# Kernel optimization log

Hardware: AMD Instinct MI355X
Metric: run time of the kernel (lower is better)

Reference implementation:

```python
import jax, jax.numpy as jnp
import numpy as np

H = W = 160  # grid mesh -> N = 25600 vertices
B = 4
D = 64


def _grid_mesh(h, w):
    """Triangulated grid; returns symmetric directed edge list (e0, e1), lexicographically
    sorted like np.where(adj > 0) in the original module."""
    idx = np.arange(h * w).reshape(h, w)
    v00 = idx[:-1, :-1].ravel(); v01 = idx[:-1, 1:].ravel()
    v10 = idx[1:, :-1].ravel(); v11 = idx[1:, 1:].ravel()
    faces = np.concatenate([np.stack([v00, v01, v11], 1), np.stack([v00, v11, v10], 1)], 0)
    pairs = np.concatenate([faces[:, [0, 1]], faces[:, [1, 2]], faces[:, [0, 2]]], 0)
    pairs = np.concatenate([pairs, pairs[:, ::-1]], 0)  # symmetrize (adj + adj.T)
    pairs = np.unique(pairs, axis=0)
    return pairs[:, 0].astype(np.int32), pairs[:, 1].astype(np.int32)


def setup_inputs() -> dict:
    key = jax.random.key(0)
    k1, k2 = jax.random.split(key)
    N = H * W
    e0, e1 = _grid_mesh(H, W)
    x = jax.random.normal(k1, (B, N, 3), dtype=jnp.float32)
    J = jax.random.normal(k2, (B, 3 * N, D), dtype=jnp.float32)
    return {"x": x, "J": J, "e0": jnp.asarray(e0), "e1": jnp.asarray(e1), "k": 0}


def _skew(v):
    # cross-product matrix [v]_x : [E,3,3]
    z = jnp.zeros_like(v[:, 0])
    return jnp.stack([
        jnp.stack([z, -v[:, 2], v[:, 1]], -1),
        jnp.stack([v[:, 2], z, -v[:, 0]], -1),
        jnp.stack([-v[:, 1], v[:, 0], z], -1)], -2)


def _arap_single(xi, Ji, e0, e1, deg):
    N = xi.shape[0]
    Dd = Ji.shape[-1]
    J3 = Ji.reshape(N, 3, Dd)           # per-node 3xD blocks of J
    v = xi[e0] - xi[e1]                  # edge vectors [E,3]
    # (2L kron I3) @ J with L = D - A (edge weights 1), coalesce == scatter-add
    nb = jnp.zeros_like(J3).at[e0].add(J3[e1])
    LJ = 2.0 * (deg[:, None, None] * J3 - nb)
    JTLJ = jnp.einsum('ncd,nce->de', J3, LJ)
    # B has block [v]_x at (e0,e1) and accumulated [v]_x at (e0,e0); B^T blocks are -[v]_x
    S = _skew(v)                         # [E,3,3]
    SJ = jnp.einsum('eij,ejd->eid', S, J3[e0])
    BTJ = jnp.zeros_like(J3).at[e1].add(-SJ).at[e0].add(-SJ)
    # C: block-diagonal, per-node sum over outgoing edges of (|v|^2 I - v v^T), then 3x3 inverse
    I3 = jnp.eye(3, dtype=xi.dtype)
    Cb = (v * v).sum(-1)[:, None, None] * I3 - v[:, :, None] * v[:, None, :]
    C = jnp.zeros((N, 3, 3), xi.dtype).at[e0].add(Cb)
    Cinv = jnp.linalg.inv(C)
    CBTJ = jnp.einsum('nij,njd->nid', Cinv, BTJ)
    JTBCBTJ = jnp.einsum('ncd,nce->de', BTJ, CBTJ)
    e = jnp.clip(jnp.linalg.eigvalsh(JTLJ - JTBCBTJ), 0.0)
    pos = e > 0
    # sqrt(clip(e,0)) with a guard so the vjp stays finite at clipped zeros
    return jnp.where(pos, jnp.sqrt(jnp.where(pos, e, 1.0)), 0.0).sum()


def reference(x, J, e0, e1, k):
    N = x.shape[1]
    deg = jnp.zeros((N,), x.dtype).at[e0].add(1.0)
    traces = jax.vmap(lambda xi, Ji: _arap_single(xi, Ji, e0, e1, deg))(x, J)
    return traces.mean()
```

## Files before the change

kernel.cpp:

```cpp
#include <hip/hip_runtime.h>

constexpr int BN = 4;
constexpr int NV = 25600;
constexpr int DD = 64;
constexpr int PP = 72;
constexpr int KP = 34;
constexpr int WW = 160;
constexpr int NPART = 8;
constexpr size_t GEOM_OFF = 1u << 20;
constexpr int GREC = 36;
constexpr int GXN  = 256;
constexpr int NCH  = NV / 4;
constexpr int NITER = NCH / GXN;
static_assert(NITER * GXN == NCH, "grid must divide chunks");

constexpr int NS_STEPS = 11;
__constant__ const float S_TAB[NS_STEPS]  = {1.999940f, 1.999730f, 1.998790f, 1.994560f,
                                             1.976020f, 1.900200f, 1.653000f, 1.241700f,
                                             1.024220f, 1.000220f, 1.000000f};
__constant__ const float MU_TAB[NS_STEPS] = {1.414192f, 1.414118f, 1.413786f, 1.412289f,
                                             1.405710f, 1.378478f, 1.285690f, 1.114316f,
                                             1.012038f, 1.000110f, 1.000000f};

typedef __attribute__((ext_vector_type(8))) short short8;
typedef __attribute__((ext_vector_type(4))) float floatx4;

__device__ __forceinline__ unsigned short f2bf(float x) {
    unsigned u = __float_as_uint(x);
    u += 0x7fffu + ((u >> 16) & 1u);
    return (unsigned short)(u >> 16);
}
__device__ __forceinline__ float bf2f(unsigned short h) {
    return __uint_as_float(((unsigned)h) << 16);
}
__device__ __forceinline__ unsigned pack2bf(float a, float b) {
    return (unsigned)f2bf(a) | ((unsigned)f2bf(b) << 16);
}

__device__ __forceinline__ void mm_arith(int n, int* mm) {
    const int r = n / WW;
    const int c = n - r * WW;
    const bool up = r > 0, dn = r < WW - 1, lf = c > 0, rt = c < WW - 1;
    mm[0] = (up && lf) ? n - WW - 1 : n;
    mm[1] = up ? n - WW : n;
    mm[2] = lf ? n - 1 : n;
    mm[3] = rt ? n + 1 : n;
    mm[4] = dn ? n + WW : n;
    mm[5] = (dn && rt) ? n + WW + 1 : n;
}

__global__ void rowptr_kernel(const int* __restrict__ e0, int E, int* __restrict__ row_ptr,
                              float* __restrict__ M, float* __restrict__ out) {
    const int i = blockIdx.x * blockDim.x + threadIdx.x;
    const int nthr = gridDim.x * blockDim.x;
    for (int j = i; j < NPART * BN * 4096; j += nthr) M[j] = 0.f;
    if (i == 0) out[0] = 0.f;
    if (i > NV) return;
    int lo = 0, hi = E;
    while (lo < hi) {
        int mid = (lo + hi) >> 1;
        if (e0[mid] < i) lo = mid + 1; else hi = mid;
    }
    row_ptr[i] = lo;
}

__global__ __launch_bounds__(256) void geom_kernel(
    const float* __restrict__ x, float* __restrict__ geom,
    float* __restrict__ M, float* __restrict__ out)
{
    const int gid = blockIdx.x * 256 + threadIdx.x;
    for (int i = gid; i < NPART * BN * 4096; i += BN * NV) M[i] = 0.f;
    if (gid == 0) out[0] = 0.f;
    if (gid >= BN * NV) return;
    const int b = gid / NV;
    const int n = gid - b * NV;
    int mm[6];
    mm_arith(n, mm);

    const float* xb = x + (size_t)b * NV * 3;
    const float xn0 = xb[n * 3], xn1 = xb[n * 3 + 1], xn2 = xb[n * 3 + 2];
    float v[6][3];
    float sv0 = 0, sv1 = 0, sv2 = 0;
    float cxx = 0, cxy = 0, cxz = 0, cyy = 0, cyz = 0, czz = 0;
#pragma unroll
    for (int k = 0; k < 6; k++) {
        const int m = mm[k];
        const float v0 = xn0 - xb[m * 3];
        const float v1 = xn1 - xb[m * 3 + 1];
        const float v2 = xn2 - xb[m * 3 + 2];
        v[k][0] = v0; v[k][1] = v1; v[k][2] = v2;
        sv0 += v0; sv1 += v1; sv2 += v2;
        const float s2 = v0 * v0 + v1 * v1 + v2 * v2;
        cxx += s2 - v0 * v0; cyy += s2 - v1 * v1; czz += s2 - v2 * v2;
        cxy -= v0 * v1; cxz -= v0 * v2; cyz -= v1 * v2;
    }
    const float co00 = cyy * czz - cyz * cyz;
    const float co01 = cxz * cyz - cxy * czz;
    const float co02 = cxy * cyz - cxz * cyy;
    const float det  = cxx * co00 + cxy * co01 + cxz * co02;
    const float id   = 1.0f / det;
    const float i00 = co00 * id, i01 = co01 * id, i02 = co02 * id;
    const float i11 = (cxx * czz - cxz * cxz) * id;
    const float i12 = (cxz * cxy - cxx * cyz) * id;
    const float i22 = (cxx * cyy - cxy * cxy) * id;

    float4* g4 = (float4*)(geom + (size_t)gid * GREC);
    g4[0] = make_float4(v[0][0], v[0][1], v[0][2], v[1][0]);
    g4[1] = make_float4(v[1][1], v[1][2], v[2][0], v[2][1]);
    g4[2] = make_float4(v[2][2], v[3][0], v[3][1], v[3][2]);
    g4[3] = make_float4(v[4][0], v[4][1], v[4][2], v[5][0]);
    g4[4] = make_float4(v[5][1], v[5][2], sv0, sv1);
    g4[5] = make_float4(sv2, i00, i01, i02);
    g4[6] = make_float4(i11, i12, i22, 0.f);
    g4[7] = make_float4(__int_as_float(mm[0]), __int_as_float(mm[1]),
                        __int_as_float(mm[2]), __int_as_float(mm[3]));
    g4[8] = make_float4(__int_as_float(mm[4]), __int_as_float(mm[5]), 0.f, 0.f);
}

__device__ __forceinline__ short8 ldfrag(const unsigned short* a, int row, int quad) {
    const unsigned* p = (const unsigned*)(a + row * KP + quad * 8);
    union { unsigned u[4]; short8 s; } t;
    t.u[0] = p[0]; t.u[1] = p[1]; t.u[2] = p[2]; t.u[3] = p[3];
    return t.s;
}

struct GRec { float v[18]; float sv[3]; float ci[6]; };
struct JRegs { float n0, n1, n2; float m0[6], m1[6], m2[6]; };

__device__ __forceinline__ void load_grec(const float* __restrict__ g, GRec& o) {
#pragma unroll
    for (int i = 0; i < 18; i++) o.v[i] = g[i];
    o.sv[0] = g[18]; o.sv[1] = g[19]; o.sv[2] = g[20];
#pragma unroll
    for (int i = 0; i < 6; i++) o.ci[i] = g[21 + i];
}

__device__ __forceinline__ void load_jregs(const float* __restrict__ Jb, int n,
                                           const int* __restrict__ mm, int lane, JRegs& o) {
    const float* Jn = Jb + (size_t)n * (3 * DD) + lane;
    o.n0 = Jn[0]; o.n1 = Jn[DD]; o.n2 = Jn[2 * DD];
#pragma unroll
    for (int k = 0; k < 6; k++) {
        const float* Jm = Jb + (size_t)mm[k] * (3 * DD) + lane;
        o.m0[k] = Jm[0]; o.m1[k] = Jm[DD]; o.m2[k] = Jm[2 * DD];
    }
}

__global__ __launch_bounds__(256, 4) void node_kernel_fast(
    const float* __restrict__ J, const float* __restrict__ geom,
    float* __restrict__ M)
{
    const int b    = blockIdx.y;
    const int w    = __builtin_amdgcn_readfirstlane(threadIdx.x >> 6);
    const int lane = threadIdx.x & 63;
    const int quad = lane >> 4;
    const int mrow = lane & 15;
    const int r0   = w * 16;

    __shared__ unsigned short ATh[2][64 * KP];
    __shared__ unsigned short BTh[2][64 * KP];
    for (int i = threadIdx.x; i < 2 * 64 * KP; i += 256) {
        (&ATh[0][0])[i] = 0;
        (&BTh[0][0])[i] = 0;
    }

    const floatx4 zero4 = {0.f, 0.f, 0.f, 0.f};
    floatx4 accM[4];
#pragma unroll
    for (int c = 0; c < 4; c++) accM[c] = zero4;

    const float* Jb = J + (size_t)b * 3 * NV * DD;
    const float* Gb = geom + (size_t)b * NV * GREC;

    GRec G0, G1;
    JRegs JA, JB;
    {
        const int n0 = blockIdx.x * 4 + w;
        int mm0[6];
        mm_arith(n0, mm0);
        load_jregs(Jb, n0, mm0, lane, JA);
        load_grec(Gb + (size_t)n0 * GREC, G0);
    }
    __syncthreads();

    auto body = [&](int it, const GRec& Gc, const JRegs& Jc, GRec& Gn, JRegs& Jnx) {
        const int p   = it & 1;
        const int itN = (it + 1 < NITER) ? (it + 1) : 0;
        const int nN  = (blockIdx.x + itN * GXN) * 4 + w;
        int mmN[6];
        mm_arith(nN, mmN);
        load_jregs(Jb, nN, mmN, lane, Jnx);
        load_grec(Gb + (size_t)nN * GREC, Gn);

        const float sm0 = (Jc.m0[0] + Jc.m0[1]) + (Jc.m0[2] + Jc.m0[3]) + (Jc.m0[4] + Jc.m0[5]);
        const float sm1 = (Jc.m1[0] + Jc.m1[1]) + (Jc.m1[2] + Jc.m1[3]) + (Jc.m1[4] + Jc.m1[5]);
        const float sm2 = (Jc.m2[0] + Jc.m2[1]) + (Jc.m2[2] + Jc.m2[3]) + (Jc.m2[4] + Jc.m2[5]);
        const float lj0 = 12.f * Jc.n0 - 2.f * sm0;
        const float lj1 = 12.f * Jc.n1 - 2.f * sm1;
        const float lj2 = 12.f * Jc.n2 - 2.f * sm2;

        const float sv0 = Gc.sv[0], sv1 = Gc.sv[1], sv2 = Gc.sv[2];
        float bt0 = sv2 * Jc.n1 - sv1 * Jc.n2;
        float bt1 = sv0 * Jc.n2 - sv2 * Jc.n0;
        float bt2 = sv1 * Jc.n0 - sv0 * Jc.n1;
#pragma unroll
        for (int k = 0; k < 6; k++) {
            const float v0 = Gc.v[k * 3], v1 = Gc.v[k * 3 + 1], v2 = Gc.v[k * 3 + 2];
            bt0 += v1 * Jc.m2[k] - v2 * Jc.m1[k];
            bt1 += v2 * Jc.m0[k] - v0 * Jc.m2[k];
            bt2 += v0 * Jc.m1[k] - v1 * Jc.m0[k];
        }

        const float i00 = Gc.ci[0], i01 = Gc.ci[1], i02 = Gc.ci[2];
        const float i11 = Gc.ci[3], i12 = Gc.ci[4], i22 = Gc.ci[5];
        const float cb0 = i00 * bt0 + i01 * bt1 + i02 * bt2;
        const float cb1 = i01 * bt0 + i11 * bt1 + i12 * bt2;
        const float cb2 = i02 * bt0 + i12 * bt1 + i22 * bt2;

        {
            const int base = lane * (KP / 2) + w * 3;
            unsigned* A32 = (unsigned*)ATh[p];
            unsigned* B32 = (unsigned*)BTh[p];
            A32[base + 0] = pack2bf(Jc.n0, Jc.n1);
            A32[base + 1] = pack2bf(Jc.n2, bt0);
            A32[base + 2] = pack2bf(bt1, bt2);
            B32[base + 0] = pack2bf(lj0, lj1);
            B32[base + 1] = pack2bf(lj2, -cb0);
            B32[base + 2] = pack2bf(-cb1, -cb2);
        }

        __syncthreads();

        const short8 ah = ldfrag(ATh[p], r0 + mrow, quad);
#pragma unroll
        for (int c = 0; c < 4; c++) {
            const short8 bh = ldfrag(BTh[p], c * 16 + mrow, quad);
            accM[c] = __builtin_amdgcn_mfma_f32_16x16x32_bf16(ah, bh, accM[c], 0, 0, 0);
        }
    };

    for (int it = 0; it < NITER - 1; it += 2) {
        body(it,     G0, JA, G1, JB);
        body(it + 1, G1, JB, G0, JA);
    }
    body(NITER - 1, G0, JA, G1, JB);

    const int prt = blockIdx.x & (NPART - 1);
    float* Mb = M + ((size_t)prt * BN + b) * 4096;
    const int cofs = blockIdx.x & 3;
#pragma unroll
    for (int cc = 0; cc < 4; cc++) {
        const int c = (cc + cofs) & 3;
#pragma unroll
        for (int r = 0; r < 4; r++)
            atomicAdd(&Mb[(r0 + quad * 4 + r) * 64 + (c * 16 + mrow)], accM[c][r]);
    }
}

__global__ __launch_bounds__(256, 4) void node_kernel_slow(
    const float* __restrict__ x, const float* __restrict__ J,
    const int* __restrict__ e1, const int* __restrict__ row_ptr,
    float* __restrict__ M)
{
    const int b    = blockIdx.y;
    const int w    = __builtin_amdgcn_readfirstlane(threadIdx.x >> 6);
    const int lane = threadIdx.x & 63;
    const int quad = lane >> 4;
    const int mrow = lane & 15;
    const int r0   = w * 16;

    __shared__ unsigned short ATh[64 * KP], ATl[64 * KP];
    __shared__ unsigned short BTh[64 * KP], BTl[64 * KP];
    for (int i = threadIdx.x; i < 64 * KP; i += 256) { ATh[i]=0; ATl[i]=0; BTh[i]=0; BTl[i]=0; }
    __syncthreads();

    const floatx4 zero4 = {0.f, 0.f, 0.f, 0.f};
    floatx4 accM[4];
#pragma unroll
    for (int c = 0; c < 4; c++) accM[c] = zero4;

    const float* xb = x + (size_t)b * NV * 3;
    const float* Jb = J + (size_t)b * 3 * NV * DD;

    for (int chunk = blockIdx.x; chunk < NV / 4; chunk += gridDim.x) {
        const int n   = chunk * 4 + w;
        const int beg = row_ptr[n];
        const int deg = row_ptr[n + 1] - beg;
        int mm[6];
#pragma unroll
        for (int k = 0; k < 6; k++) {
            const int idx = beg + ((k < deg) ? k : 0);
            const int mv  = e1[idx];
            mm[k] = (k < deg) ? mv : n;
        }
        const float* Jn = Jb + n * 3 * DD + lane;
        const float jn0 = Jn[0], jn1 = Jn[DD], jn2 = Jn[2 * DD];
        float jm0[6], jm1[6], jm2[6];
#pragma unroll
        for (int k = 0; k < 6; k++) {
            const float* Jm = Jb + mm[k] * 3 * DD + lane;
            jm0[k] = Jm[0]; jm1[k] = Jm[DD]; jm2[k] = Jm[2 * DD];
        }
        const float xn0 = xb[n * 3 + 0], xn1 = xb[n * 3 + 1], xn2 = xb[n * 3 + 2];
        float va0[6], va1[6], va2[6];
#pragma unroll
        for (int k = 0; k < 6; k++) {
            va0[k] = xn0 - xb[mm[k] * 3 + 0];
            va1[k] = xn1 - xb[mm[k] * 3 + 1];
            va2[k] = xn2 - xb[mm[k] * 3 + 2];
        }
        float lj0=0, lj1=0, lj2=0, bt0=0, bt1=0, bt2=0;
        float cxx=0, cxy=0, cxz=0, cyy=0, cyz=0, czz=0;
#pragma unroll
        for (int k = 0; k < 6; k++) {
            const float v0 = va0[k], v1 = va1[k], v2 = va2[k];
            const float t0 = jm0[k]-jn0, t1 = jm1[k]-jn1, t2 = jm2[k]-jn2;
            lj0 -= t0; lj1 -= t1; lj2 -= t2;
            bt0 += v1*t2 - v2*t1; bt1 += v2*t0 - v0*t2; bt2 += v0*t1 - v1*t0;
            const float s2 = v0*v0 + v1*v1 + v2*v2;
            cxx += s2 - v0*v0; cyy += s2 - v1*v1; czz += s2 - v2*v2;
            cxy -= v0*v1; cxz -= v0*v2; cyz -= v1*v2;
        }
        lj0 *= 2.f; lj1 *= 2.f; lj2 *= 2.f;
        const float co00 = cyy*czz - cyz*cyz;
        const float co01 = cxz*cyz - cxy*czz;
        const float co02 = cxy*cyz - cxz*cyy;
        const float det  = cxx*co00 + cxy*co01 + cxz*co02;
        const float id   = 1.0f / det;
        const float i00 = co00*id, i01 = co01*id, i02 = co02*id;
        const float i11 = (cxx*czz - cxz*cxz)*id;
        const float i12 = (cxz*cxy - cxx*cyz)*id;
        const float i22 = (cxx*cyy - cxy*cxy)*id;
        const float cb0 = i00*bt0 + i01*bt1 + i02*bt2;
        const float cb1 = i01*bt0 + i11*bt1 + i12*bt2;
        const float cb2 = i02*bt0 + i12*bt1 + i22*bt2;
        {
            const int kA = w * 6;
            float av[6] = {jn0, jn1, jn2, bt0, bt1, bt2};
            float bv[6] = {lj0, lj1, lj2, -cb0, -cb1, -cb2};
#pragma unroll
            for (int i = 0; i < 6; i++) {
                unsigned short h = f2bf(av[i]);
                ATh[lane*KP + kA + i] = h; ATl[lane*KP + kA + i] = f2bf(av[i] - bf2f(h));
                h = f2bf(bv[i]);
                BTh[lane*KP + kA + i] = h; BTl[lane*KP + kA + i] = f2bf(bv[i] - bf2f(h));
            }
        }
        __syncthreads();
        const short8 ah = ldfrag(ATh, r0 + mrow, quad);
        const short8 al = ldfrag(ATl, r0 + mrow, quad);
#pragma unroll
        for (int c = 0; c < 4; c++) {
            const short8 bh = ldfrag(BTh, c*16 + mrow, quad);
            const short8 bl = ldfrag(BTl, c*16 + mrow, quad);
            accM[c] = __builtin_amdgcn_mfma_f32_16x16x32_bf16(ah, bh, accM[c], 0, 0, 0);
            accM[c] = __builtin_amdgcn_mfma_f32_16x16x32_bf16(ah, bl, accM[c], 0, 0, 0);
            accM[c] = __builtin_amdgcn_mfma_f32_16x16x32_bf16(al, bh, accM[c], 0, 0, 0);
        }
        __syncthreads();
    }
    const int prt = blockIdx.x & (NPART - 1);
    float* Mb = M + ((size_t)prt * BN + b) * 4096;
#pragma unroll
    for (int c = 0; c < 4; c++)
#pragma unroll
        for (int r = 0; r < 4; r++)
            atomicAdd(&Mb[(r0 + quad*4 + r) * 64 + (c*16 + mrow)], accM[c][r]);
}

__global__ __launch_bounds__(1024, 1) void ns_sqrt_kernel(const float* __restrict__ M,
                                                          float* __restrict__ out)
{
    const int b    = blockIdx.x;
    const int tid  = threadIdx.x;
    const int w    = tid >> 6;
    const int lane = tid & 63;
    const int quad = lane >> 4;
    const int mrow = lane & 15;
    const int tr   = (w & 3) * 16;
    const int tc   = (w >> 2) * 16;

    __shared__ __align__(16) unsigned short Yh[2][64 * PP], Yl[2][64 * PP];
    __shared__ __align__(16) unsigned short Zh[2][64 * PP], Zl[2][64 * PP];
    __shared__ __align__(16) unsigned short Wh[64 * PP], Wl[64 * PP];
    __shared__ float msum[4096];
    __shared__ float red_s[16];
    __shared__ float tr_s;

    constexpr int PS = BN * 4096;
    const float* Mb = M + b * 4096;

    {
        float f2 = 0.f;
        for (int i = tid; i < 4096; i += 1024) {
            float v = 0.f;
#pragma unroll
            for (int pI = 0; pI < NPART; pI++) v += Mb[pI * PS + i];
            msum[i] = v;
            f2 += v * v;
        }
#pragma unroll
        for (int off = 32; off; off >>= 1) f2 += __shfl_down(f2, off, 64);
        if (lane == 0) red_s[w] = f2;
        if (tid < 64) {
            float d = 0.f;
#pragma unroll
            for (int pI = 0; pI < NPART; pI++) d += Mb[pI * PS + tid * 65];
#pragma unroll
            for (int off = 32; off; off >>= 1) d += __shfl_down(d, off, 64);
            if (tid == 0) tr_s = d;
        }
    }
    __syncthreads();
    const float trM   = tr_s;
    float f2s = 0.f;
#pragma unroll
    for (int i = 0; i < 16; i++) f2s += red_s[i];
    const float fro   = sqrtf(f2s);
    const float delta = 3e-5f * trM;
    const float cnorm = fro + 2.f * delta;
    const float inv_c = 1.f / cnorm;

    {
        const float s0 = S_TAB[0], mu0 = MU_TAB[0];
        for (int i = tid; i < 4096; i += 1024) {
            const int r = i >> 6, col = i & 63;
            float y = msum[i] * inv_c;
            if (r == col) y += delta * inv_c;
            unsigned short h = f2bf(y);
            Yh[0][r * PP + col] = h;
            Yl[0][r * PP + col] = f2bf(y - bf2f(h));
            float wv = mu0 * (-0.5f * s0 * y);
            if (r == col) wv += mu0 * 1.5f;
            h = f2bf(wv);
            Wh[r * PP + col] = h;
            Wl[r * PP + col] = f2bf(wv - bf2f(h));
            Zh[1][r * PP + col] = h;
            Zl[1][r * PP + col] = Wl[r * PP + col];
        }
    }
    __syncthreads();

    const floatx4 zero4 = {0.f, 0.f, 0.f, 0.f};

    {
        floatx4 y0 = zero4, y1 = zero4, y2 = zero4;
#pragma unroll
        for (int ks = 0; ks < 2; ks++) {
            const int ko = ks * 32 + quad * 8;
            const short8 yah = *(const short8*)&Yh[0][(tr + mrow) * PP + ko];
            const short8 yal = *(const short8*)&Yl[0][(tr + mrow) * PP + ko];
            const short8 wbh = *(const short8*)&Wh[(tc + mrow) * PP + ko];
            const short8 wbl = *(const short8*)&Wl[(tc + mrow) * PP + ko];
            y0 = __builtin_amdgcn_mfma_f32_16x16x32_bf16(yah, wbh, y0, 0, 0, 0);
            y1 = __builtin_amdgcn_mfma_f32_16x16x32_bf16(yah, wbl, y1, 0, 0, 0);
            y2 = __builtin_amdgcn_mfma_f32_16x16x32_bf16(yal, wbh, y2, 0, 0, 0);
        }
#pragma unroll
        for (int r = 0; r < 4; r++) {
            const int row = tr + quad * 4 + r;
            const int col = tc + mrow;
            const float vy = y0[r] + y1[r] + y2[r];
            const unsigned short h = f2bf(vy);
            Yh[1][row * PP + col] = h;
            Yl[1][row * PP + col] = f2bf(vy - bf2f(h));
        }
        __syncthreads();
    }

    for (int it = 1; it < NS_STEPS; ++it) {
        const int cur = it & 1, nxt = cur ^ 1;
        const float s = S_TAB[it], mu = MU_TAB[it];
        const unsigned short* yh = Yh[cur]; const unsigned short* yl = Yl[cur];
        const unsigned short* zh = Zh[cur]; const unsigned short* zl = Zl[cur];

        floatx4 t0 = zero4, t1 = zero4, t2 = zero4;
#pragma unroll
        for (int ks = 0; ks < 2; ks++) {
            const int ko = ks * 32 + quad * 8;
            const short8 zah = *(const short8*)&zh[(tr + mrow) * PP + ko];
            const short8 zal = *(const short8*)&zl[(tr + mrow) * PP + ko];
            const short8 ybh = *(const short8*)&yh[(tc + mrow) * PP + ko];
            const short8 ybl = *(const short8*)&yl[(tc + mrow) * PP + ko];
            t0 = __builtin_amdgcn_mfma_f32_16x16x32_bf16(zah, ybh, t0, 0, 0, 0);
            t1 = __builtin_amdgcn_mfma_f32_16x16x32_bf16(zah, ybl, t1, 0, 0, 0);
            t2 = __builtin_amdgcn_mfma_f32_16x16x32_bf16(zal, ybh, t2, 0, 0, 0);
        }
#pragma unroll
        for (int r = 0; r < 4; r++) {
            const int row = tr + quad * 4 + r;
            const int col = tc + mrow;
            float v = mu * (-0.5f * s) * (t0[r] + t1[r] + t2[r]);
            if (row == col) v += mu * 1.5f;
            const unsigned short h = f2bf(v);
            Wh[row * PP + col] = h;
            Wl[row * PP + col] = f2bf(v - bf2f(h));
        }
        __syncthreads();

        floatx4 y0 = zero4, y1 = zero4, y2 = zero4, z0 = zero4, z1 = zero4, z2 = zero4;
#pragma unroll
        for (int ks = 0; ks < 2; ks++) {
            const int ko = ks * 32 + quad * 8;
            const int ar = (tr + mrow) * PP + ko;
            const int bc = (tc + mrow) * PP + ko;
            const short8 yah = *(const short8*)&yh[ar];
            const short8 yal = *(const short8*)&yl[ar];
            const short8 wah = *(const short8*)&Wh[ar];
            const short8 wal = *(const short8*)&Wl[ar];
            const short8 wbh = *(const short8*)&Wh[bc];
            const short8 wbl = *(const short8*)&Wl[bc];
            const short8 zbh = *(const short8*)&zh[bc];
            const short8 zbl = *(const short8*)&zl[bc];
            y0 = __builtin_amdgcn_mfma_f32_16x16x32_bf16(yah, wbh, y0, 0, 0, 0);
            y1 = __builtin_amdgcn_mfma_f32_16x16x32_bf16(yah, wbl, y1, 0, 0, 0);
            y2 = __builtin_amdgcn_mfma_f32_16x16x32_bf16(yal, wbh, y2, 0, 0, 0);
            z0 = __builtin_amdgcn_mfma_f32_16x16x32_bf16(wah, zbh, z0, 0, 0, 0);
            z1 = __builtin_amdgcn_mfma_f32_16x16x32_bf16(wah, zbl, z1, 0, 0, 0);
            z2 = __builtin_amdgcn_mfma_f32_16x16x32_bf16(wal, zbh, z2, 0, 0, 0);
        }
#pragma unroll
        for (int r = 0; r < 4; r++) {
            const int row = tr + quad * 4 + r;
            const int col = tc + mrow;
            const float vy = y0[r] + y1[r] + y2[r];
            const float vz = z0[r] + z1[r] + z2[r];
            unsigned short h = f2bf(vy);
            Yh[nxt][row * PP + col] = h;
            Yl[nxt][row * PP + col] = f2bf(vy - bf2f(h));
            h = f2bf(vz);
            Zh[nxt][row * PP + col] = h;
            Zl[nxt][row * PP + col] = f2bf(vz - bf2f(h));
        }
        __syncthreads();
    }

    const int fin = NS_STEPS & 1;
    if (tid < 64) {
        float d = bf2f(Yh[fin][tid * PP + tid]) + bf2f(Yl[fin][tid * PP + tid]);
#pragma unroll
        for (int off = 32; off; off >>= 1) d += __shfl_down(d, off, 64);
        if (tid == 0) atomicAdd(out, d * sqrtf(cnorm) * (1.0f / BN));
    }
}

extern "C" void kernel_launch(void* const* d_in, const int* in_sizes, int n_in,
                              void* d_out, int out_size, void* d_ws, size_t ws_size,
                              hipStream_t stream) {
    const float* x  = (const float*)d_in[0];
    const float* J  = (const float*)d_in[1];
    const int*   e0 = (const int*)d_in[2];
    const int*   e1 = (const int*)d_in[3];
    const int E = in_sizes[2];

    int*   row_ptr = (int*)d_ws;
    float* M       = (float*)((char*)d_ws + 128 * 1024);
    float* geom    = (float*)((char*)d_ws + GEOM_OFF);
    const size_t need = GEOM_OFF + (size_t)BN * NV * GREC * sizeof(float);

    if (ws_size >= need) {
        geom_kernel<<<(BN * NV + 255) / 256, 256, 0, stream>>>(x, geom, M, (float*)d_out);
        node_kernel_fast<<<dim3(GXN, BN), 256, 0, stream>>>(J, geom, M);
    } else {
        rowptr_kernel<<<(NV + 1 + 255) / 256, 256, 0, stream>>>(e0, E, row_ptr, M, (float*)d_out);
        node_kernel_slow<<<dim3(512, BN), 256, 0, stream>>>(x, J, e1, row_ptr, M);
    }
    ns_sqrt_kernel<<<BN, 1024, 0, stream>>>(M, (float*)d_out);
}
```

Baseline: 188.2 us.

## Deepen node-kernel prefetch to two stages, assign contiguous chunks, and shrink geom records

The node kernel now keeps three register sets for geometry and J and prefetches two iterations ahead instead of one, to hide more global-load latency. Each block now walks a contiguous range of chunks (with a swizzled block index) rather than striding by the grid size, which should improve neighbour-row reuse in cache. The geometry record drops the unused neighbour-index fields (36 to 28 floats), and bf16 packing uses the hardware v_cvt_pk_bf16_f32 instruction. The extra register sets raise VGPR pressure under the 256x4 launch bound and may cause spills or lower occupancy.

```diff
diff --git a/kernel.cpp b/kernel.cpp
--- a/kernel.cpp
+++ b/kernel.cpp
@@ -8,7 +8,7 @@
 constexpr int WW = 160;
 constexpr int NPART = 8;
 constexpr size_t GEOM_OFF = 1u << 20;
-constexpr int GREC = 36;
+constexpr int GREC = 28;
 constexpr int GXN  = 256;
 constexpr int NCH  = NV / 4;
 constexpr int NITER = NCH / GXN;
@@ -34,7 +34,9 @@
     return __uint_as_float(((unsigned)h) << 16);
 }
 __device__ __forceinline__ unsigned pack2bf(float a, float b) {
-    return (unsigned)f2bf(a) | ((unsigned)f2bf(b) << 16);
+    unsigned r;
+    asm("v_cvt_pk_bf16_f32 %0, %1, %2" : "=v"(r) : "v"(a), "v"(b));
+    return r;
 }
 
 __device__ __forceinline__ void mm_arith(int n, int* mm) {
@@ -112,9 +114,6 @@
     g4[4] = make_float4(v[5][1], v[5][2], sv0, sv1);
     g4[5] = make_float4(sv2, i00, i01, i02);
     g4[6] = make_float4(i11, i12, i22, 0.f);
-    g4[7] = make_float4(__int_as_float(mm[0]), __int_as_float(mm[1]),
-                        __int_as_float(mm[2]), __int_as_float(mm[3]));
-    g4[8] = make_float4(__int_as_float(mm[4]), __int_as_float(mm[5]), 0.f, 0.f);
 }
 
 __device__ __forceinline__ short8 ldfrag(const unsigned short* a, int row, int quad) {
@@ -156,6 +155,8 @@
     const int quad = lane >> 4;
     const int mrow = lane & 15;
     const int r0   = w * 16;
+    const int bxs  = (blockIdx.x & 7) * (GXN / 8) + (blockIdx.x >> 3);
+    const int ch0  = bxs * NITER;
 
     __shared__ unsigned short ATh[2][64 * KP];
     __shared__ unsigned short BTh[2][64 * KP];
@@ -172,25 +173,29 @@
     const float* Jb = J + (size_t)b * 3 * NV * DD;
     const float* Gb = geom + (size_t)b * NV * GREC;
 
-    GRec G0, G1;
-    JRegs JA, JB;
+    GRec G0, G1, G2;
+    JRegs J0, J1, J2;
     {
-        const int n0 = blockIdx.x * 4 + w;
         int mm0[6];
-        mm_arith(n0, mm0);
-        load_jregs(Jb, n0, mm0, lane, JA);
-        load_grec(Gb + (size_t)n0 * GREC, G0);
+        const int na = (ch0 + 0) * 4 + w;
+        mm_arith(na, mm0);
+        load_jregs(Jb, na, mm0, lane, J0);
+        load_grec(Gb + (size_t)na * GREC, G0);
+        const int nb2 = (ch0 + 1) * 4 + w;
+        mm_arith(nb2, mm0);
+        load_jregs(Jb, nb2, mm0, lane, J1);
+        load_grec(Gb + (size_t)nb2 * GREC, G1);
     }
     __syncthreads();
 
-    auto body = [&](int it, const GRec& Gc, const JRegs& Jc, GRec& Gn, JRegs& Jnx) {
+    auto body = [&](int it, const GRec& Gc, const JRegs& Jc, GRec& Gp, JRegs& Jp) {
         const int p   = it & 1;
-        const int itN = (it + 1 < NITER) ? (it + 1) : 0;
-        const int nN  = (blockIdx.x + itN * GXN) * 4 + w;
-        int mmN[6];
-        mm_arith(nN, mmN);
-        load_jregs(Jb, nN, mmN, lane, Jnx);
-        load_grec(Gb + (size_t)nN * GREC, Gn);
+        const int itP = (it + 2 < NITER) ? (it + 2) : 0;
+        const int nP  = (ch0 + itP) * 4 + w;
+        int mmP[6];
+        mm_arith(nP, mmP);
+        load_jregs(Jb, nP, mmP, lane, Jp);
+        load_grec(Gb + (size_t)nP * GREC, Gp);
 
         const float sm0 = (Jc.m0[0] + Jc.m0[1]) + (Jc.m0[2] + Jc.m0[3]) + (Jc.m0[4] + Jc.m0[5]);
         const float sm1 = (Jc.m1[0] + Jc.m1[1]) + (Jc.m1[2] + Jc.m1[3]) + (Jc.m1[4] + Jc.m1[5]);
@@ -239,11 +244,12 @@
         }
     };
 
-    for (int it = 0; it < NITER - 1; it += 2) {
-        body(it,     G0, JA, G1, JB);
-        body(it + 1, G1, JB, G0, JA);
-    }
-    body(NITER - 1, G0, JA, G1, JB);
+    for (int it = 0; it < NITER - 1; it += 3) {
+        body(it,     G0, J0, G2, J2);
+        body(it + 1, G1, J1, G0, J0);
+        body(it + 2, G2, J2, G1, J1);
+    }
+    body(NITER - 1, G0, J0, G2, J2);
 
     const int prt = blockIdx.x & (NPART - 1);
     float* Mb = M + ((size_t)prt * BN + b) * 4096;
```

New measurement: 182.2 us. 3.2% less time.
